# Kernel optimization log

Measured on AMD Instinct MI355X. Metric: run time of the kernel, lower is better.

The kernel has to match this reference:

```python
import jax, jax.numpy as jnp
import numpy as np

TIME = 10  # hardcoded interpolation steps in the original module


def _interpolation(poly, time=TIME):
    # poly: [B, N, 2] -> [B, N*time, 2]
    poly_roll = jnp.roll(poly, shift=1, axis=1)
    step = (jnp.arange(time, dtype=poly.dtype) / time)[:, None]        # [T, 1]
    # [B, N, T, 2] = current * step + previous * (1 - step)
    interp = poly[:, :, None, :] * step + poly_roll[:, :, None, :] * (1.0 - step)
    return interp.reshape(poly.shape[0], -1, 2)


def _compute_distance(pred_poly, gt_poly):
    # pred_poly: [B, Np, 2], gt_poly: [B, Ng, 2] -> squared dists [B, Ng, Np]
    diff = gt_poly[:, :, None, :] - pred_poly[:, None, :, :]
    return jnp.sum(diff * diff, axis=3)


def reference(ini_pred_poly, pred_polys_, gt_polys, keyPointsMask):
    # --- lossPred2NearestGt: each pred point matched to nearest interpolated gt ---
    gt_interp = _interpolation(gt_polys)                               # [B, Ng*T, 2]
    dist_pg = _compute_distance(ini_pred_poly, gt_interp)              # [B, Ng*T, Np]
    index_gt = jnp.argmin(dist_pg, axis=1)                             # [B, Np]
    nearest_gt = jnp.take_along_axis(gt_interp, index_gt[:, :, None], axis=1)  # [B, Np, 2]
    loss_pred2gt = jnp.mean(jnp.abs(pred_polys_ - nearest_gt))         # l1, mean reduction

    # --- lossGt2NearestPred: each gt vertex matched to nearest pred point ---
    dist_gp = _compute_distance(ini_pred_poly, gt_polys)               # [B, Ng, Np]
    index_pred = jnp.argmin(dist_gp, axis=2)                           # [B, Ng]
    nearest_pred = jnp.take_along_axis(pred_polys_, index_pred[:, :, None], axis=1)  # [B, Ng, 2]
    loss_gt2pred = jnp.abs(nearest_pred - gt_polys)                    # l1, no reduction, [B, Ng, 2]

    mask = jnp.broadcast_to(keyPointsMask[:, :, None], loss_gt2pred.shape)
    loss = jnp.sum(loss_gt2pred * mask) / (jnp.sum(mask) + 1.0) + loss_pred2gt
    return loss / 2.0


def setup_inputs() -> dict:
    key = jax.random.key(0)
    k1, k2, k3, k4 = jax.random.split(key, 4)
    B, Np, Ng = 1024, 128, 128
    return {
        "ini_pred_poly": jax.random.uniform(k1, (B, Np, 2), dtype=jnp.float32),
        "pred_polys_": jax.random.uniform(k2, (B, Np, 2), dtype=jnp.float32),
        "gt_polys": jax.random.uniform(k3, (B, Ng, 2), dtype=jnp.float32),
        "keyPointsMask": jax.random.uniform(k4, (B, Ng), dtype=jnp.float32),
    }
```

## Files before the change

kernel.cpp:

```cpp
#include <hip/hip_runtime.h>


constexpr int NP = 128;
constexpr int NG = 128;

__global__ __launch_bounds__(512) void dm_main(
    const float* __restrict__ ini,
    const float* __restrict__ pp,
    const float* __restrict__ gt,
    const float* __restrict__ mask,
    float* __restrict__ partial)
{
    const int b   = blockIdx.x;
    const int tid = threadIdx.x;

    __shared__ float2 s_gt [NG];
    __shared__ float2 s_ini[NP];
    __shared__ float2 s_pp [NP];
    __shared__ float4 s_seg[NG];
    __shared__ float4 s_r1 [8][64];
    __shared__ float4 s_r2 [8][64];
    __shared__ float  s_red[6];

    const float2* gtb  = (const float2*)(gt  + (size_t)b * 256);
    const float2* inib = (const float2*)(ini + (size_t)b * 256);
    const float2* ppb  = (const float2*)(pp  + (size_t)b * 256);

    if (tid < 128) {
        const float2 cv = gtb[tid];
        const float2 pv = gtb[(tid + 127) & 127];
        s_gt [tid] = cv;
        s_seg[tid] = make_float4(pv.x, pv.y, cv.x - pv.x, cv.y - pv.y);
    } else if (tid < 256) {
        s_ini[tid - 128] = inib[tid - 128];
    } else if (tid < 384) {
        s_pp [tid - 256] = ppb[tid - 256];
    }

    const int pr = tid & 63;
    const int g  = tid >> 6;
    const float2 q0 = inib[pr];
    const float2 q1 = inib[pr + 64];
    const float2 g0 = gtb [pr];
    const float2 g1 = gtb [pr + 64];
    const float  mval = (tid < NP) ? mask[(size_t)b * NG + tid] : 0.0f;
    __syncthreads();

    {
        float bd0 = 3.4e38f, bi0 = 0.0f, bd1 = 3.4e38f, bi1 = 0.0f;
        float basef = (float)(g * 160);
        const int s0 = g * 16;
        #pragma unroll
        for (int k = 0; k < 16; ++k) {
            const float4 sg = s_seg[s0 + k];
            const float ex = sg.z, ey = sg.w;
            const float ee  = fmaxf(fmaf(ex, ex, ey * ey), 1e-30f);
            const float s10 = 10.0f * __builtin_amdgcn_rcpf(ee);
            {
                const float wx = q0.x - sg.x, wy = q0.y - sg.y;
                const float dot = fmaf(wy, ey, wx * ex);
                float tc = rintf(dot * s10);
                tc = __builtin_amdgcn_fmed3f(tc, 0.0f, 9.0f);
                const float u   = tc * 0.1f;
                const float dqx = fmaf(-u, ex, wx);
                const float dqy = fmaf(-u, ey, wy);
                const float d   = fmaf(dqy, dqy, dqx * dqx);
                const float cand = basef + tc;
                bi0 = (d < bd0) ? cand : bi0;
                bd0 = fminf(d, bd0);
            }
            {
                const float wx = q1.x - sg.x, wy = q1.y - sg.y;
                const float dot = fmaf(wy, ey, wx * ex);
                float tc = rintf(dot * s10);
                tc = __builtin_amdgcn_fmed3f(tc, 0.0f, 9.0f);
                const float u   = tc * 0.1f;
                const float dqx = fmaf(-u, ex, wx);
                const float dqy = fmaf(-u, ey, wy);
                const float d   = fmaf(dqy, dqy, dqx * dqx);
                const float cand = basef + tc;
                bi1 = (d < bd1) ? cand : bi1;
                bd1 = fminf(d, bd1);
            }
            basef += 10.0f;
        }
        s_r1[g][pr] = make_float4(bd0, bi0, bd1, bi1);
    }

    {
        float bd0 = 3.4e38f, bj0 = 0.0f, bd1 = 3.4e38f, bj1 = 0.0f;
        float jf = (float)(g * 16);
        const int j0 = g * 16;
        #pragma unroll
        for (int k = 0; k < 16; ++k) {
            const float2 pv = s_ini[j0 + k];
            {
                const float dx = g0.x - pv.x, dy = g0.y - pv.y;
                const float d  = fmaf(dy, dy, dx * dx);
                bj0 = (d < bd0) ? jf : bj0;
                bd0 = fminf(d, bd0);
            }
            {
                const float dx = g1.x - pv.x, dy = g1.y - pv.y;
                const float d  = fmaf(dy, dy, dx * dx);
                bj1 = (d < bd1) ? jf : bj1;
                bd1 = fminf(d, bd1);
            }
            jf += 1.0f;
        }
        s_r2[g][pr] = make_float4(bd0, bj0, bd1, bj1);
    }
    __syncthreads();

    float l_a = 0.0f, l_c = 0.0f, l_m = 0.0f;
    if (tid < NP) {
        const int slot = tid >> 6;
        const int ln   = tid & 63;

        float bd = 3.4e38f, bi = 0.0f;
        #pragma unroll
        for (int gg = 0; gg < 8; ++gg) {
            const float4 r  = s_r1[gg][ln];
            const float d2 = slot ? r.z : r.x;
            const float i2 = slot ? r.w : r.y;
            bi = (d2 < bd) ? i2 : bi;
            bd = fminf(d2, bd);
        }
        const int idx = (int)bi;
        const int n = idx / 10;
        const int t = idx - n * 10;
        const float step = (float)t / 10.0f;
        const float om   = 1.0f - step;
        const float2 c  = s_gt[n];
        const float2 prv = s_gt[(n + NG - 1) & (NG - 1)];
        const float nx = c.x * step + prv.x * om;
        const float ny = c.y * step + prv.y * om;
        const float2 mp = s_pp[tid];
        l_a = fabsf(mp.x - nx) + fabsf(mp.y - ny);

        float cd = 3.4e38f, cj = 0.0f;
        #pragma unroll
        for (int gg = 0; gg < 8; ++gg) {
            const float4 r  = s_r2[gg][ln];
            const float d2 = slot ? r.z : r.x;
            const float j2 = slot ? r.w : r.y;
            cj = (d2 < cd) ? j2 : cj;
            cd = fminf(d2, cd);
        }
        const float2 npt = s_pp[(int)cj];
        const float2 gvv = s_gt[tid];
        l_c = mval * (fabsf(npt.x - gvv.x) + fabsf(npt.y - gvv.y));
        l_m = 2.0f * mval;
    }

    const int wid = tid >> 6, lane = tid & 63;
    if (wid < 2) {
        for (int off = 32; off > 0; off >>= 1) {
            l_a += __shfl_down(l_a, off);
            l_c += __shfl_down(l_c, off);
            l_m += __shfl_down(l_m, off);
        }
        if (lane == 0) {
            s_red[wid * 3 + 0] = l_a;
            s_red[wid * 3 + 1] = l_c;
            s_red[wid * 3 + 2] = l_m;
        }
    }
    __syncthreads();
    if (tid == 0) {
        partial[(size_t)b * 3 + 0] = s_red[0] + s_red[3];
        partial[(size_t)b * 3 + 1] = s_red[1] + s_red[4];
        partial[(size_t)b * 3 + 2] = s_red[2] + s_red[5];
    }
}

__global__ __launch_bounds__(256) void dm_final(
    const float* __restrict__ partial, int nb, double inv_count, float* __restrict__ out)
{
    const int tid = threadIdx.x;
    double a = 0.0, c = 0.0, d = 0.0;
    for (int b = tid; b < nb; b += 256) {
        a += (double)partial[(size_t)b * 3 + 0];
        c += (double)partial[(size_t)b * 3 + 1];
        d += (double)partial[(size_t)b * 3 + 2];
    }
    for (int off = 32; off > 0; off >>= 1) {
        a += __shfl_down(a, off);
        c += __shfl_down(c, off);
        d += __shfl_down(d, off);
    }
    __shared__ double s[12];
    const int wid = tid >> 6, lane = tid & 63;
    if (lane == 0) { s[wid * 3] = a; s[wid * 3 + 1] = c; s[wid * 3 + 2] = d; }
    __syncthreads();
    if (tid == 0) {
        const double at = s[0] + s[3] + s[6] + s[9];
        const double ct = s[1] + s[4] + s[7] + s[10];
        const double dt = s[2] + s[5] + s[8] + s[11];
        const double loss = ct / (dt + 1.0) + at * inv_count;
        out[0] = (float)(loss * 0.5);
    }
}

extern "C" void kernel_launch(void* const* d_in, const int* in_sizes, int n_in,
                              void* d_out, int out_size, void* d_ws, size_t ws_size,
                              hipStream_t stream) {
    const float* ini  = (const float*)d_in[0];
    const float* pp   = (const float*)d_in[1];
    const float* gt   = (const float*)d_in[2];
    const float* mask = (const float*)d_in[3];
    float* out = (float*)d_out;

    const int B = in_sizes[0] / (NP * 2);
    float* partial = (float*)d_ws;

    dm_main<<<B, 512, 0, stream>>>(ini, pp, gt, mask, partial);
    const double inv_count = 1.0 / ((double)B * NP * 2);
    dm_final<<<1, 256, 0, stream>>>(partial, B, inv_count, out);
}
```

Before: 20.56 us.

## Fuse final reduction into main kernel via fixed-point atomics and last-block finish

Removes the separate single-block reduction kernel. Each block now atomically adds fixed-point 64-bit partial sums to a workspace, and the last block to arrive (tracked by an atomic ticket) computes the final loss. The two per-point argmin reductions are also split across two waves instead of running serially in one. This adds a memset launch and a global atomic per block, and it depends on the ordering between the partial-sum atomics and the ticket atomic, which has no explicit fence.

```diff
diff --git a/kernel.cpp b/kernel.cpp
--- a/kernel.cpp
+++ b/kernel.cpp
@@ -4,12 +4,13 @@
 constexpr int NP = 128;
 constexpr int NG = 128;
 
-__global__ __launch_bounds__(512) void dm_main(
+__global__ __launch_bounds__(512) void dm_fused(
     const float* __restrict__ ini,
     const float* __restrict__ pp,
     const float* __restrict__ gt,
     const float* __restrict__ mask,
-    float* __restrict__ partial)
+    unsigned long long* __restrict__ acc,
+    float* __restrict__ out, int nblocks, double inv_count)
 {
     const int b   = blockIdx.x;
     const int tid = threadIdx.x;
@@ -43,7 +44,7 @@
     const float2 q1 = inib[pr + 64];
     const float2 g0 = gtb [pr];
     const float2 g1 = gtb [pr + 64];
-    const float  mval = (tid < NP) ? mask[(size_t)b * NG + tid] : 0.0f;
+    const float  mval = (tid < 256) ? mask[(size_t)b * NG + (tid & 127)] : 0.0f;
     __syncthreads();
 
     {
@@ -58,28 +59,24 @@
             const float s10 = 10.0f * __builtin_amdgcn_rcpf(ee);
             {
                 const float wx = q0.x - sg.x, wy = q0.y - sg.y;
-                const float dot = fmaf(wy, ey, wx * ex);
-                float tc = rintf(dot * s10);
+                float tc = rintf(fmaf(wy, ey, wx * ex) * s10);
                 tc = __builtin_amdgcn_fmed3f(tc, 0.0f, 9.0f);
                 const float u   = tc * 0.1f;
                 const float dqx = fmaf(-u, ex, wx);
                 const float dqy = fmaf(-u, ey, wy);
                 const float d   = fmaf(dqy, dqy, dqx * dqx);
-                const float cand = basef + tc;
-                bi0 = (d < bd0) ? cand : bi0;
+                bi0 = (d < bd0) ? (basef + tc) : bi0;
                 bd0 = fminf(d, bd0);
             }
             {
                 const float wx = q1.x - sg.x, wy = q1.y - sg.y;
-                const float dot = fmaf(wy, ey, wx * ex);
-                float tc = rintf(dot * s10);
+                float tc = rintf(fmaf(wy, ey, wx * ex) * s10);
                 tc = __builtin_amdgcn_fmed3f(tc, 0.0f, 9.0f);
                 const float u   = tc * 0.1f;
                 const float dqx = fmaf(-u, ex, wx);
                 const float dqy = fmaf(-u, ey, wy);
                 const float d   = fmaf(dqy, dqy, dqx * dqx);
-                const float cand = basef + tc;
-                bi1 = (d < bd1) ? cand : bi1;
+                bi1 = (d < bd1) ? (basef + tc) : bi1;
                 bd1 = fminf(d, bd1);
             }
             basef += 10.0f;
@@ -113,10 +110,9 @@
     __syncthreads();
 
     float l_a = 0.0f, l_c = 0.0f, l_m = 0.0f;
-    if (tid < NP) {
+    if (tid < 128) {
         const int slot = tid >> 6;
         const int ln   = tid & 63;
-
         float bd = 3.4e38f, bi = 0.0f;
         #pragma unroll
         for (int gg = 0; gg < 8; ++gg) {
@@ -131,13 +127,16 @@
         const int t = idx - n * 10;
         const float step = (float)t / 10.0f;
         const float om   = 1.0f - step;
-        const float2 c  = s_gt[n];
+        const float2 c   = s_gt[n];
         const float2 prv = s_gt[(n + NG - 1) & (NG - 1)];
         const float nx = c.x * step + prv.x * om;
         const float ny = c.y * step + prv.y * om;
         const float2 mp = s_pp[tid];
         l_a = fabsf(mp.x - nx) + fabsf(mp.y - ny);
-
+    } else if (tid < 256) {
+        const int v    = tid - 128;
+        const int slot = v >> 6;
+        const int ln   = v & 63;
         float cd = 3.4e38f, cj = 0.0f;
         #pragma unroll
         for (int gg = 0; gg < 8; ++gg) {
@@ -148,57 +147,41 @@
             cd = fminf(d2, cd);
         }
         const float2 npt = s_pp[(int)cj];
-        const float2 gvv = s_gt[tid];
+        const float2 gvv = s_gt[v];
         l_c = mval * (fabsf(npt.x - gvv.x) + fabsf(npt.y - gvv.y));
         l_m = 2.0f * mval;
     }
 
     const int wid = tid >> 6, lane = tid & 63;
     if (wid < 2) {
+        for (int off = 32; off > 0; off >>= 1) l_a += __shfl_down(l_a, off);
+        if (lane == 0) s_red[wid] = l_a;
+    } else if (wid < 4) {
         for (int off = 32; off > 0; off >>= 1) {
-            l_a += __shfl_down(l_a, off);
             l_c += __shfl_down(l_c, off);
             l_m += __shfl_down(l_m, off);
         }
-        if (lane == 0) {
-            s_red[wid * 3 + 0] = l_a;
-            s_red[wid * 3 + 1] = l_c;
-            s_red[wid * 3 + 2] = l_m;
-        }
+        if (lane == 0) { s_red[2 * wid - 2] = l_c; s_red[2 * wid - 1] = l_m; }
     }
     __syncthreads();
+
     if (tid == 0) {
-        partial[(size_t)b * 3 + 0] = s_red[0] + s_red[3];
-        partial[(size_t)b * 3 + 1] = s_red[1] + s_red[4];
-        partial[(size_t)b * 3 + 2] = s_red[2] + s_red[5];
-    }
-}
-
-__global__ __launch_bounds__(256) void dm_final(
-    const float* __restrict__ partial, int nb, double inv_count, float* __restrict__ out)
-{
-    const int tid = threadIdx.x;
-    double a = 0.0, c = 0.0, d = 0.0;
-    for (int b = tid; b < nb; b += 256) {
-        a += (double)partial[(size_t)b * 3 + 0];
-        c += (double)partial[(size_t)b * 3 + 1];
-        d += (double)partial[(size_t)b * 3 + 2];
-    }
-    for (int off = 32; off > 0; off >>= 1) {
-        a += __shfl_down(a, off);
-        c += __shfl_down(c, off);
-        d += __shfl_down(d, off);
-    }
-    __shared__ double s[12];
-    const int wid = tid >> 6, lane = tid & 63;
-    if (lane == 0) { s[wid * 3] = a; s[wid * 3 + 1] = c; s[wid * 3 + 2] = d; }
-    __syncthreads();
-    if (tid == 0) {
-        const double at = s[0] + s[3] + s[6] + s[9];
-        const double ct = s[1] + s[4] + s[7] + s[10];
-        const double dt = s[2] + s[5] + s[8] + s[11];
-        const double loss = ct / (dt + 1.0) + at * inv_count;
-        out[0] = (float)(loss * 0.5);
+        const double FPS = 4294967296.0;
+        const double a = (double)s_red[0] + (double)s_red[1];
+        const double c = (double)s_red[2] + (double)s_red[4];
+        const double m = (double)s_red[3] + (double)s_red[5];
+        unsigned long long o0 = atomicAdd(&acc[0], (unsigned long long)llrint(a * FPS));
+        unsigned long long o1 = atomicAdd(&acc[1], (unsigned long long)llrint(c * FPS));
+        unsigned long long o2 = atomicAdd(&acc[2], (unsigned long long)llrint(m * FPS));
+        asm volatile("" :: "v"(o0), "v"(o1), "v"(o2) : "memory");
+        const unsigned long long tick = atomicAdd(&acc[3], 1ull);
+        if (tick == (unsigned long long)(nblocks - 1)) {
+            const double at = (double)atomicAdd(&acc[0], 0ull) / FPS;
+            const double ct = (double)atomicAdd(&acc[1], 0ull) / FPS;
+            const double mt = (double)atomicAdd(&acc[2], 0ull) / FPS;
+            const double loss = ct / (mt + 1.0) + at * inv_count;
+            out[0] = (float)(loss * 0.5);
+        }
     }
 }
 
@@ -209,12 +192,12 @@
     const float* pp   = (const float*)d_in[1];
     const float* gt   = (const float*)d_in[2];
     const float* mask = (const float*)d_in[3];
-    float* out = (float*)d_out;
 
     const int B = in_sizes[0] / (NP * 2);
-    float* partial = (float*)d_ws;
-
-    dm_main<<<B, 512, 0, stream>>>(ini, pp, gt, mask, partial);
+    unsigned long long* acc = (unsigned long long*)d_ws;
+
+    hipMemsetAsync(d_ws, 0, 4 * sizeof(unsigned long long), stream);
+
     const double inv_count = 1.0 / ((double)B * NP * 2);
-    dm_final<<<1, 256, 0, stream>>>(partial, B, inv_count, out);
+    dm_fused<<<B, 512, 0, stream>>>(ini, pp, gt, mask, acc, (float*)d_out, B, inv_count);
 }
```

Result: slower. 64.65 us (+214.5%).
